# Kernel tuning notes

Measured on AMD Instinct MI355X. Metric: run time of the kernel, lower is better.

The kernel has to match this reference:

```python
import jax, jax.numpy as jnp
import numpy as np

NUM_HEADS = 16
NUM_GROUPS = 4
NUM_KV_HEADS = NUM_HEADS // NUM_GROUPS  # 4
HEAD_DIM = 64
MAX_DIST = 484


def setup_inputs() -> dict:
    key = jax.random.key(0)
    ks = jax.random.split(key, 8)
    B, S, E, H = 32, 484, 1024, 1024
    kv_dim = HEAD_DIM * NUM_GROUPS  # 256
    s_in = 0.03
    return {
        "query": jax.random.normal(ks[0], (B, S, E), dtype=jnp.float32),
        "key": jax.random.normal(ks[1], (B, S, E), dtype=jnp.float32),
        "value": jax.random.normal(ks[2], (B, S, E), dtype=jnp.float32),
        "Wq": jax.random.normal(ks[3], (E, H), dtype=jnp.float32) * s_in,
        "Wk": jax.random.normal(ks[4], (E, kv_dim), dtype=jnp.float32) * s_in,
        "Wv": jax.random.normal(ks[5], (E, kv_dim), dtype=jnp.float32) * s_in,
        "Wo": jax.random.normal(ks[6], (H, E), dtype=jnp.float32) * s_in,
        "rel_table": jax.random.normal(ks[7], (2 * MAX_DIST - 1, NUM_HEADS), dtype=jnp.float32) * 0.02,
    }


def _rel_bias(rel_table, q_len, k_len):
    # relative position k - q, clipped to [-(MD-1), MD-1], shifted to table index
    rel = jnp.arange(k_len)[None, :] - jnp.arange(q_len)[:, None]
    idx = jnp.clip(rel, -(MAX_DIST - 1), MAX_DIST - 1) + (MAX_DIST - 1)
    bias = rel_table[idx]  # [q, k, heads]
    return jnp.transpose(bias, (2, 0, 1))  # [heads, q, k]


def reference(query, key, value, Wq, Wk, Wv, Wo, rel_table):
    B, Q, _ = query.shape
    K = key.shape[1]
    G, Hkv, D = NUM_GROUPS, NUM_KV_HEADS, HEAD_DIM
    # projections; torch head split: head index = g*Hkv + h
    q = (query @ Wq).reshape(B, Q, G * Hkv, D).transpose(0, 2, 1, 3)
    q = q.reshape(B, G, Hkv, Q, D)  # b g h sq d
    k = (key @ Wk).reshape(B, K, G, D).transpose(0, 2, 1, 3)  # b g sk d
    v = (value @ Wv).reshape(B, K, G, D).transpose(0, 2, 1, 3)  # b g sv d
    scale = jnp.float32(D) ** 0.5
    scores = jnp.einsum('bghqd,bgkd->bghqk', q, k) / scale
    bias = _rel_bias(rel_table, Q, K).reshape(1, G, Hkv, Q, K)
    attn = jax.nn.softmax(scores + bias, axis=-1)
    out = jnp.einsum('bghqk,bgkd->bghqd', attn, v)
    out = out.reshape(B, G * Hkv, Q, D).transpose(0, 2, 1, 3).reshape(B, Q, G * Hkv * D)
    return out @ Wo
```

## Files before the change

### kernel.cpp

```cpp
#include <hip/hip_runtime.h>
#include <hip/hip_bf16.h>

typedef __attribute__((ext_vector_type(8))) short short8;
typedef __attribute__((ext_vector_type(4))) float f32x4;
typedef __attribute__((ext_vector_type(4))) unsigned uintx4;

#define B_  32
#define S_  484
#define E_  1024
#define NH  16
#define SP  512
#define M_  (B_*S_)

static __device__ __forceinline__ ushort f2bf(float f) {
  union { float f; unsigned u; } v; v.f = f;
  unsigned u = v.u;
  return (ushort)((u + 0x7FFFu + ((u >> 16) & 1u)) >> 16);
}

static __device__ __forceinline__ unsigned cvt_pk_bf16(float lo, float hi) {
  unsigned r;
  asm("v_cvt_pk_bf16_f32 %0, %1, %2" : "=v"(r) : "v"(lo), "v"(hi));
  return r;
}

#define GLOAD_LDS16(gp, lp) \
  __builtin_amdgcn_global_load_lds((const __attribute__((address_space(1))) void*)(gp), \
                                   (__attribute__((address_space(3))) void*)(lp), 16, 0, 0)

__global__ __launch_bounds__(256)
void transpose_convert(const float* __restrict__ W, ushort* __restrict__ WT, int K, int N) {
  __shared__ float tile[32][33];
  int k0 = blockIdx.y * 32, n0 = blockIdx.x * 32;
  int tx = threadIdx.x, ty = threadIdx.y;
  for (int i = ty; i < 32; i += 8) tile[i][tx] = W[(size_t)(k0 + i) * N + n0 + tx];
  __syncthreads();
  for (int i = ty; i < 32; i += 8) WT[(size_t)(n0 + i) * K + k0 + tx] = f2bf(tile[tx][i]);
}

template<int EPI, int SWZ, int AF32, int NXLOG>
__global__ __launch_bounds__(256)
void gemm_bt(const void* __restrict__ Ain, const ushort* __restrict__ BT,
             void* __restrict__ Cout, int N, int K, int HN, float oscale) {
  __shared__ alignas(16) ushort sA[2][128 * 32];
  __shared__ alignas(16) ushort sB[2][128 * 32];
  const int tid = threadIdx.x;
  const int lane = tid & 63, w = tid >> 6;

  const int nwg = gridDim.x;
  const int qq = nwg >> 3, rr = nwg & 7;
  const int x = blockIdx.x & 7, seq = blockIdx.x >> 3;
  const int logical = x * qq + (x < rr ? x : rr) + seq;
  const int m0 = (logical >> NXLOG) * 128;
  const int n0 = (logical & ((1 << NXLOG) - 1)) * 128;
  const int NK = K >> 5;

  const int srow = w * 32 + (lane >> 2);
  const int scol = (lane & 3) * 8;
  const ushort* gB0 = BT + (size_t)(n0 + srow) * K + scol;

  const ushort* gA0bf = (const ushort*)Ain + (size_t)(m0 + srow) * K + scol;
  const int arow = w * 32 + (lane >> 1);
  const int acol = (lane & 1) * 16;
  const float* gA0f = (const float*)Ain + (size_t)(m0 + arow) * K + acol;

  const int wr = w >> 1, wc = w & 1;
  const int g4 = lane >> 4, l16 = lane & 15;
  const int aoff = (wr * 64 + l16) * 32 + 8 * g4;
  const int boff = (wc * 64 + l16) * 32 + 8 * g4;

  f32x4 acc[4][4] = {};
  float4 fA0, fA1, fA2, fA3;

  auto issueA = [&](int kt) {
    const float4* p = (const float4*)(gA0f + kt * 32);
    fA0 = p[0]; fA1 = p[1]; fA2 = p[2]; fA3 = p[3];
  };
  auto writeA = [&](int buf) {
    unsigned d0 = cvt_pk_bf16(fA0.x, fA0.y), d1 = cvt_pk_bf16(fA0.z, fA0.w);
    unsigned d2 = cvt_pk_bf16(fA1.x, fA1.y), d3 = cvt_pk_bf16(fA1.z, fA1.w);
    unsigned d4 = cvt_pk_bf16(fA2.x, fA2.y), d5 = cvt_pk_bf16(fA2.z, fA2.w);
    unsigned d6 = cvt_pk_bf16(fA3.x, fA3.y), d7 = cvt_pk_bf16(fA3.z, fA3.w);
    ushort* dst = &sA[buf][arow * 32 + acol];
    uintx4 q0 = {d0, d1, d2, d3}, q1 = {d4, d5, d6, d7};
    *(uintx4*)dst = q0;
    *(uintx4*)(dst + 8) = q1;
  };

  if (AF32) issueA(0);
  else {
    GLOAD_LDS16(gA0bf,          &sA[0][(w * 32) * 32]);
    GLOAD_LDS16(gA0bf + 16 * K, &sA[0][(w * 32 + 16) * 32]);
  }
  GLOAD_LDS16(gB0,          &sB[0][(w * 32) * 32]);
  GLOAD_LDS16(gB0 + 16 * K, &sB[0][(w * 32 + 16) * 32]);
  if (AF32) writeA(0);

  for (int kt = 0; kt < NK; ++kt) {
    __syncthreads();
    const int nb = (kt + 1) & 1;
    if (kt + 1 < NK) {
      const ushort* gb = gB0 + (kt + 1) * 32;
      GLOAD_LDS16(gb,          &sB[nb][(w * 32) * 32]);
      GLOAD_LDS16(gb + 16 * K, &sB[nb][(w * 32 + 16) * 32]);
      if (AF32) issueA(kt + 1);
      else {
        const ushort* ga = gA0bf + (kt + 1) * 32;
        GLOAD_LDS16(ga,          &sA[nb][(w * 32) * 32]);
        GLOAD_LDS16(ga + 16 * K, &sA[nb][(w * 32 + 16) * 32]);
      }
    }
    const ushort* pa = &sA[kt & 1][aoff];
    const ushort* pb = &sB[kt & 1][boff];
    short8 af[4], bf[4];
#pragma unroll
    for (int i = 0; i < 4; ++i) {
      af[i] = *(const short8*)(pa + i * 16 * 32);
      bf[i] = *(const short8*)(pb + i * 16 * 32);
    }
#pragma unroll
    for (int mi = 0; mi < 4; ++mi)
#pragma unroll
      for (int ni = 0; ni < 4; ++ni)
        acc[mi][ni] = __builtin_amdgcn_mfma_f32_16x16x32_bf16(af[mi], bf[ni], acc[mi][ni], 0, 0, 0);
    if (AF32 && kt + 1 < NK) writeA(nb);
  }

#pragma unroll
  for (int mi = 0; mi < 4; ++mi) {
#pragma unroll
    for (int ni = 0; ni < 4; ++ni) {
#pragma unroll
      for (int r = 0; r < 4; ++r) {
        int m = m0 + wr * 64 + mi * 16 + g4 * 4 + r;
        int n = n0 + wc * 64 + ni * 16 + l16;
        float vv = acc[mi][ni][r];
        if (EPI == 2) {
          ((float*)Cout)[(size_t)m * N + n] = vv;
        } else {
          int b = m / S_, pos = m % S_;
          if (EPI == 0) {
            int dd = n & 63;
            if (SWZ) dd ^= (pos & 7) << 3;
            ushort hv = f2bf(vv * oscale);
            ((ushort*)Cout)[(((size_t)b * HN + (n >> 6)) * SP + pos) * 64 + dd] = hv;
          } else {
            int local = pos & 31;
            int j = (local < 16) ? (2 * local) : (2 * local - 31);
            int pf_ = (pos & ~31) | (j ^ ((n & 3) << 3));
            ushort hv = f2bf(vv);
            ((ushort*)Cout)[(((size_t)b * HN + (n >> 6)) * 64 + (n & 63)) * SP + pf_] = hv;
          }
        }
      }
    }
  }
}

__global__ __launch_bounds__(256)
void attn_kernel(const ushort* __restrict__ qp, const ushort* __restrict__ kp,
                 const ushort* __restrict__ vpT, const float* __restrict__ rel,
                 ushort* __restrict__ ao) {
  __shared__ float sBias[1056];
  __shared__ alignas(16) ushort sK[2][32 * 64];
  __shared__ alignas(16) ushort sV[2][64 * 32];
  __shared__ alignas(16) ushort sP[4][16 * 40];
  const int tid = threadIdx.x;
  const int blk = blockIdx.x;
  const int logical = (blk & 7) * 512 + (blk >> 3);
  const int qt = logical & 7, head = (logical >> 3) & 15, b = logical >> 7;
  const int g = head >> 2;
  const float LOG2E = 1.44269504f;
  for (int t = tid; t < 1056; t += 256)
    sBias[t] = (t >= 32 && t < 999) ? rel[(t - 32) * 16 + head] * LOG2E : -1e30f;

  const int lane = tid & 63, w = tid >> 6;
  const int g4 = lane >> 4, l16 = lane & 15;
  const int qw = qt * 64 + w * 16;

  const ushort* qbase = qp + (((size_t)b * NH + head) * SP + qw + l16) * 64;
  short8 qf0 = *(const short8*)(qbase + 8 * g4);
  short8 qf1 = *(const short8*)(qbase + 32 + 8 * g4);

  const ushort* kSrc = kp  + ((size_t)b * 4 + g) * SP * 64 + (tid >> 3) * 64 + (tid & 7) * 8;
  const ushort* vSrc = vpT + ((size_t)b * 4 + g) * 64 * SP + (tid >> 2) * SP + (tid & 3) * 8;

  f32x4 acc[4] = {};
  float ps[4] = {0.f, 0.f, 0.f, 0.f};
  const int ib = l16 - (qw + g4 * 4) + 483 + 32;
  ushort* sPw = &sP[w][0];

  const int kswz  = (l16 & 7) << 3;
  const int kOff0 = l16 * 64 + ((8 * g4) ^ kswz);
  const int kOff1 = l16 * 64 + ((32 + 8 * g4) ^ kswz);
  const int vOff  = l16 * 32 + 8 * (g4 ^ (l16 & 3));

  GLOAD_LDS16(kSrc, &sK[0][w * 512]);
  GLOAD_LDS16(vSrc, &sV[0][w * 512]);

  for (int kt = 0; kt < 16; ++kt) {
    __syncthreads();
    if (kt + 1 < 16) {
      GLOAD_LDS16(kSrc + (kt + 1) * 2048, &sK[(kt + 1) & 1][w * 512]);
      GLOAD_LDS16(vSrc + (kt + 1) * 32,   &sV[(kt + 1) & 1][w * 512]);
    }
    const ushort* sk = &sK[kt & 1][0];
    const ushort* sv = &sV[kt & 1][0];
    short8 kf0 = *(const short8*)(sk + kOff0);
    short8 kf1 = *(const short8*)(sk + kOff1);
    short8 kf2 = *(const short8*)(sk + 1024 + kOff0);
    short8 kf3 = *(const short8*)(sk + 1024 + kOff1);
    f32x4 s0 = {}, s1 = {};
    s0 = __builtin_amdgcn_mfma_f32_16x16x32_bf16(qf0, kf0, s0, 0, 0, 0);
    s0 = __builtin_amdgcn_mfma_f32_16x16x32_bf16(qf1, kf1, s0, 0, 0, 0);
    s1 = __builtin_amdgcn_mfma_f32_16x16x32_bf16(qf0, kf2, s1, 0, 0, 0);
    s1 = __builtin_amdgcn_mfma_f32_16x16x32_bf16(qf1, kf3, s1, 0, 0, 0);

    const int k0 = kt * 32;
#pragma unroll
    for (int r = 0; r < 4; ++r) {
      int i0 = ib + k0 - r;
      float p0 = __builtin_amdgcn_exp2f(s0[r] + sBias[i0]);
      float p1 = __builtin_amdgcn_exp2f(s1[r] + sBias[i0 + 16]);
      if (kt == 15) {
        p0 = (k0 + l16 < S_) ? p0 : 0.f;
        p1 = (k0 + 16 + l16 < S_) ? p1 : 0.f;
      }
      ps[r] += p0 + p1;
      *(unsigned*)(sPw + (g4 * 4 + r) * 40 + 2 * l16) = cvt_pk_bf16(p0, p1);
    }
    short8 pf = *(const short8*)(sPw + l16 * 40 + 8 * g4);
#pragma unroll
    for (int nt = 0; nt < 4; ++nt) {
      short8 vf = *(const short8*)(sv + vOff + nt * 512);
      acc[nt] = __builtin_amdgcn_mfma_f32_16x16x32_bf16(pf, vf, acc[nt], 0, 0, 0);
    }
  }

#pragma unroll
  for (int off = 1; off < 16; off <<= 1) {
#pragma unroll
    for (int r = 0; r < 4; ++r) ps[r] += __shfl_xor(ps[r], off, 64);
  }

#pragma unroll
  for (int r = 0; r < 4; ++r) {
    int q_abs = qw + g4 * 4 + r;
    if (q_abs < S_) {
      float inv = 1.f / ps[r];
#pragma unroll
      for (int nt = 0; nt < 4; ++nt) {
        int dd = nt * 16 + l16;
        ao[((size_t)b * S_ + q_abs) * 1024 + head * 64 + dd] = f2bf(acc[nt][r] * inv);
      }
    }
  }
}

extern "C" void kernel_launch(void* const* d_in, const int* in_sizes, int n_in,
                              void* d_out, int out_size, void* d_ws, size_t ws_size,
                              hipStream_t stream) {
  const float* query = (const float*)d_in[0];
  const float* key   = (const float*)d_in[1];
  const float* value = (const float*)d_in[2];
  const float* Wq    = (const float*)d_in[3];
  const float* Wk    = (const float*)d_in[4];
  const float* Wv    = (const float*)d_in[5];
  const float* Wo    = (const float*)d_in[6];
  const float* rel   = (const float*)d_in[7];

  char* ws = (char*)d_ws;
  size_t off = 0;
  auto alloc = [&](size_t bytes) { char* p = ws + off; off += (bytes + 255) & ~(size_t)255; return p; };

  const size_t MEelems = (size_t)M_ * E_;
  ushort* wqT = (ushort*)alloc((size_t)1024 * 1024 * 2);
  ushort* wkT = (ushort*)alloc((size_t)256 * 1024 * 2);
  ushort* wvT = (ushort*)alloc((size_t)256 * 1024 * 2);
  ushort* woT = (ushort*)alloc((size_t)1024 * 1024 * 2);
  ushort* qp  = (ushort*)alloc((size_t)B_ * NH * SP * 64 * 2);
  ushort* kp  = (ushort*)alloc((size_t)B_ * 4 * SP * 64 * 2);
  ushort* vp  = (ushort*)alloc((size_t)B_ * 4 * 64 * SP * 2);
  ushort* ao  = (ushort*)alloc(MEelems * 2);

  transpose_convert<<<dim3(32, 32), dim3(32, 8), 0, stream>>>(Wq, wqT, 1024, 1024);
  transpose_convert<<<dim3(8, 32),  dim3(32, 8), 0, stream>>>(Wk, wkT, 1024, 256);
  transpose_convert<<<dim3(8, 32),  dim3(32, 8), 0, stream>>>(Wv, wvT, 1024, 256);
  transpose_convert<<<dim3(32, 32), dim3(32, 8), 0, stream>>>(Wo, woT, 1024, 1024);

  const float QSCALE = 0.125f * 1.44269504f;
  gemm_bt<0,0,1,3><<<968, 256, 0, stream>>>(query, wqT, qp, 1024, 1024, NH, QSCALE);
  gemm_bt<0,1,1,1><<<242, 256, 0, stream>>>(key,   wkT, kp, 256, 1024, 4, 1.0f);
  gemm_bt<1,1,1,1><<<242, 256, 0, stream>>>(value, wvT, vp, 256, 1024, 4, 1.0f);

  attn_kernel<<<4096, 256, 0, stream>>>(qp, kp, vp, rel, ao);

  gemm_bt<2,0,0,3><<<968, 256, 0, stream>>>(ao, woT, d_out, 1024, 1024, 0, 1.0f);
}
```

Baseline: 305.6 us.

## Use 256x256-tile GEMM kernel with 512 threads for Q and output projections

Adds a gemm_big kernel that computes 256x256 output tiles with 8 waves, each holding an 8x4 grid of MFMA accumulators, and uses it for the Q projection and the output projection. Larger tiles cut global and LDS traffic per FLOP and halve the redundant fp32 A reloads. The cost is 244 workgroups on a 256-CU device, higher register pressure from 128 accumulator floats per lane, and a partial last M tile that needs bounds checks. The EPI==2 branch is dropped from gemm_bt because it is no longer used.

New measurement: 301.8 us. About the same (-1.2%).

```diff
diff --git a/kernel.cpp b/kernel.cpp
--- a/kernel.cpp
+++ b/kernel.cpp
@@ -36,6 +36,106 @@
   for (int i = ty; i < 32; i += 8) tile[i][tx] = W[(size_t)(k0 + i) * N + n0 + tx];
   __syncthreads();
   for (int i = ty; i < 32; i += 8) WT[(size_t)(n0 + i) * K + k0 + tx] = f2bf(tile[tx][i]);
+}
+
+template<int EPI, int AF32>
+__global__ __launch_bounds__(512)
+void gemm_big(const void* __restrict__ Ain, const ushort* __restrict__ BT,
+              void* __restrict__ Cout, float oscale) {
+  const int K = 1024, N = 1024, NK = 32;
+  __shared__ alignas(16) ushort sA[2][256 * 32];
+  __shared__ alignas(16) ushort sB[2][256 * 32];
+  const int tid = threadIdx.x;
+  const int lane = tid & 63, w = tid >> 6;
+  const int m0 = (blockIdx.x >> 2) * 256;
+  const int n0 = (blockIdx.x & 3) * 256;
+
+  const int brow = tid >> 2, bcol = (tid & 3) * 8;
+  const ushort* gB0 = BT + (size_t)(n0 + brow) * K + bcol;
+  const int dstB = tid * 8;
+
+  const int rowA0 = min(m0 + brow, M_ - 1);
+  const int rowA1 = min(m0 + brow + 128, M_ - 1);
+  const ushort* gA0bf = (const ushort*)Ain + (size_t)rowA0 * K + bcol;
+  const ushort* gA1bf = (const ushort*)Ain + (size_t)rowA1 * K + bcol;
+
+  const int rowAf = min(m0 + (tid >> 1), M_ - 1);
+  const float* gA0f = (const float*)Ain + (size_t)rowAf * K + (tid & 1) * 16;
+  const int dstAf = (tid >> 1) * 32 + (tid & 1) * 16;
+
+  const int wr = w >> 2, wc = w & 3;
+  const int g4 = lane >> 4, l16 = lane & 15;
+
+  f32x4 acc[8][4] = {};
+  float4 fA0, fA1, fA2, fA3;
+
+  auto issueA = [&](int kt) {
+    const float4* p = (const float4*)(gA0f + kt * 32);
+    fA0 = p[0]; fA1 = p[1]; fA2 = p[2]; fA3 = p[3];
+  };
+  auto writeA = [&](int buf) {
+    unsigned d0 = cvt_pk_bf16(fA0.x, fA0.y), d1 = cvt_pk_bf16(fA0.z, fA0.w);
+    unsigned d2 = cvt_pk_bf16(fA1.x, fA1.y), d3 = cvt_pk_bf16(fA1.z, fA1.w);
+    unsigned d4 = cvt_pk_bf16(fA2.x, fA2.y), d5 = cvt_pk_bf16(fA2.z, fA2.w);
+    unsigned d6 = cvt_pk_bf16(fA3.x, fA3.y), d7 = cvt_pk_bf16(fA3.z, fA3.w);
+    ushort* dst = &sA[buf][dstAf];
+    uintx4 q0 = {d0, d1, d2, d3}, q1 = {d4, d5, d6, d7};
+    *(uintx4*)dst = q0;
+    *(uintx4*)(dst + 8) = q1;
+  };
+  auto stage = [&](int kt, int buf) {
+    GLOAD_LDS16(gB0 + kt * 32,           &sB[buf][dstB]);
+    GLOAD_LDS16(gB0 + kt * 32 + 128 * K, &sB[buf][dstB + 4096]);
+    if (AF32) issueA(kt);
+    else {
+      GLOAD_LDS16(gA0bf + kt * 32, &sA[buf][dstB]);
+      GLOAD_LDS16(gA1bf + kt * 32, &sA[buf][dstB + 4096]);
+    }
+  };
+
+  stage(0, 0);
+  if (AF32) writeA(0);
+
+  for (int kt = 0; kt < NK; ++kt) {
+    __syncthreads();
+    const int nb = (kt + 1) & 1;
+    if (kt + 1 < NK) stage(kt + 1, nb);
+    const ushort* pa = &sA[kt & 1][(wr * 128 + l16) * 32 + 8 * g4];
+    const ushort* pb = &sB[kt & 1][(wc * 64 + l16) * 32 + 8 * g4];
+    short8 af[8], bf[4];
+#pragma unroll
+    for (int i = 0; i < 8; ++i) af[i] = *(const short8*)(pa + i * 16 * 32);
+#pragma unroll
+    for (int i = 0; i < 4; ++i) bf[i] = *(const short8*)(pb + i * 16 * 32);
+#pragma unroll
+    for (int mi = 0; mi < 8; ++mi)
+#pragma unroll
+      for (int ni = 0; ni < 4; ++ni)
+        acc[mi][ni] = __builtin_amdgcn_mfma_f32_16x16x32_bf16(af[mi], bf[ni], acc[mi][ni], 0, 0, 0);
+    if (AF32 && kt + 1 < NK) writeA(nb);
+  }
+
+#pragma unroll
+  for (int mi = 0; mi < 8; ++mi) {
+#pragma unroll
+    for (int ni = 0; ni < 4; ++ni) {
+#pragma unroll
+      for (int r = 0; r < 4; ++r) {
+        int m = m0 + wr * 128 + mi * 16 + g4 * 4 + r;
+        int n = n0 + wc * 64 + ni * 16 + l16;
+        if (m < M_) {
+          float vv = acc[mi][ni][r];
+          if (EPI == 2) {
+            ((float*)Cout)[(size_t)m * N + n] = vv;
+          } else {
+            int b = m / S_, pos = m % S_;
+            ushort hv = f2bf(vv * oscale);
+            ((ushort*)Cout)[(((size_t)b * NH + (n >> 6)) * SP + pos) * 64 + (n & 63)] = hv;
+          }
+        }
+      }
+    }
+  }
 }
 
 template<int EPI, int SWZ, int AF32, int NXLOG>
@@ -135,22 +235,18 @@
         int m = m0 + wr * 64 + mi * 16 + g4 * 4 + r;
         int n = n0 + wc * 64 + ni * 16 + l16;
         float vv = acc[mi][ni][r];
-        if (EPI == 2) {
-          ((float*)Cout)[(size_t)m * N + n] = vv;
+        int b = m / S_, pos = m % S_;
+        if (EPI == 0) {
+          int dd = n & 63;
+          if (SWZ) dd ^= (pos & 7) << 3;
+          ushort hv = f2bf(vv * oscale);
+          ((ushort*)Cout)[(((size_t)b * HN + (n >> 6)) * SP + pos) * 64 + dd] = hv;
         } else {
-          int b = m / S_, pos = m % S_;
-          if (EPI == 0) {
-            int dd = n & 63;
-            if (SWZ) dd ^= (pos & 7) << 3;
-            ushort hv = f2bf(vv * oscale);
-            ((ushort*)Cout)[(((size_t)b * HN + (n >> 6)) * SP + pos) * 64 + dd] = hv;
-          } else {
-            int local = pos & 31;
-            int j = (local < 16) ? (2 * local) : (2 * local - 31);
-            int pf_ = (pos & ~31) | (j ^ ((n & 3) << 3));
-            ushort hv = f2bf(vv);
-            ((ushort*)Cout)[(((size_t)b * HN + (n >> 6)) * 64 + (n & 63)) * SP + pf_] = hv;
-          }
+          int local = pos & 31;
+          int j = (local < 16) ? (2 * local) : (2 * local - 31);
+          int pf_ = (pos & ~31) | (j ^ ((n & 3) << 3));
+          ushort hv = f2bf(vv);
+          ((ushort*)Cout)[(((size_t)b * HN + (n >> 6)) * 64 + (n & 63)) * SP + pf_] = hv;
         }
       }
     }
@@ -289,11 +385,11 @@
   transpose_convert<<<dim3(32, 32), dim3(32, 8), 0, stream>>>(Wo, woT, 1024, 1024);
 
   const float QSCALE = 0.125f * 1.44269504f;
-  gemm_bt<0,0,1,3><<<968, 256, 0, stream>>>(query, wqT, qp, 1024, 1024, NH, QSCALE);
+  gemm_big<0,1><<<244, 512, 0, stream>>>(query, wqT, qp, QSCALE);
   gemm_bt<0,1,1,1><<<242, 256, 0, stream>>>(key,   wkT, kp, 256, 1024, 4, 1.0f);
   gemm_bt<1,1,1,1><<<242, 256, 0, stream>>>(value, wvT, vp, 256, 1024, 4, 1.0f);
 
   attn_kernel<<<4096, 256, 0, stream>>>(qp, kp, vp, rel, ao);
 
-  gemm_bt<2,0,0,3><<<968, 256, 0, stream>>>(ao, woT, d_out, 1024, 1024, 0, 1.0f);
-}
+  gemm_big<2,0><<<244, 512, 0, stream>>>(ao, woT, d_out, 1.0f);
+}
```

## Pre-convert query to bf16 and use triple-buffered async-LDS GEMM for Q and output projections

Applied to the files above, without the earlier changes.

Adds a standalone kernel that converts the fp32 query activations to bf16. The Q projection and output projection then run in a new GEMM that loads both operands with global_load_lds into a three-stage LDS ring, with explicit vmcnt waits, so loads run two tiles ahead of compute. The aim is to take the fp32 load and register conversion off the Q GEMM's critical path and to deepen prefetch. In exchange the query tensor takes an extra full fp32 read and bf16 write-back (about 60MB plus 30MB of traffic), and LDS use rises to 48KB per block, which may lower occupancy.

New measurement: 297.4 us. 2.7% less time.

```diff
diff --git a/kernel.cpp b/kernel.cpp
--- a/kernel.cpp
+++ b/kernel.cpp
@@ -27,6 +27,18 @@
 #define GLOAD_LDS16(gp, lp) \
   __builtin_amdgcn_global_load_lds((const __attribute__((address_space(1))) void*)(gp), \
                                    (__attribute__((address_space(3))) void*)(lp), 16, 0, 0)
+
+__global__ __launch_bounds__(256)
+void cvt_f32_bf16(const float* __restrict__ x, ushort* __restrict__ y, int n4) {
+  int i = blockIdx.x * 256 + threadIdx.x;
+  int stride = gridDim.x * 256;
+  for (; i < n4; i += stride) {
+    float4 v = ((const float4*)x)[i];
+    ushort4 h;
+    h.x = f2bf(v.x); h.y = f2bf(v.y); h.z = f2bf(v.z); h.w = f2bf(v.w);
+    ((ushort4*)y)[i] = h;
+  }
+}
 
 __global__ __launch_bounds__(256)
 void transpose_convert(const float* __restrict__ W, ushort* __restrict__ WT, int K, int N) {
@@ -38,12 +50,12 @@
   for (int i = ty; i < 32; i += 8) WT[(size_t)(n0 + i) * K + k0 + tx] = f2bf(tile[tx][i]);
 }
 
-template<int EPI, int SWZ, int AF32, int NXLOG>
-__global__ __launch_bounds__(256)
-void gemm_bt(const void* __restrict__ Ain, const ushort* __restrict__ BT,
-             void* __restrict__ Cout, int N, int K, int HN, float oscale) {
-  __shared__ alignas(16) ushort sA[2][128 * 32];
-  __shared__ alignas(16) ushort sB[2][128 * 32];
+template<int EPI, int NXLOG>
+__global__ __launch_bounds__(256)
+void gemm_cnt(const ushort* __restrict__ A, const ushort* __restrict__ BT,
+              void* __restrict__ Cout, int N, int K, float oscale) {
+  __shared__ alignas(16) ushort sA[3][128 * 32];
+  __shared__ alignas(16) ushort sB[3][128 * 32];
   const int tid = threadIdx.x;
   const int lane = tid & 63, w = tid >> 6;
 
@@ -57,12 +69,99 @@
 
   const int srow = w * 32 + (lane >> 2);
   const int scol = (lane & 3) * 8;
+  const ushort* gA0 = A  + (size_t)(m0 + srow) * K + scol;
   const ushort* gB0 = BT + (size_t)(n0 + srow) * K + scol;
 
-  const ushort* gA0bf = (const ushort*)Ain + (size_t)(m0 + srow) * K + scol;
+  const int wr = w >> 1, wc = w & 1;
+  const int g4 = lane >> 4, l16 = lane & 15;
+  const int aoff = (wr * 64 + l16) * 32 + 8 * g4;
+  const int boff = (wc * 64 + l16) * 32 + 8 * g4;
+
+  f32x4 acc[4][4] = {};
+
+  auto stage = [&](int kt, int buf) {
+    const ushort* ga = gA0 + kt * 32;
+    const ushort* gb = gB0 + kt * 32;
+    GLOAD_LDS16(ga,          &sA[buf][(w * 32) * 32]);
+    GLOAD_LDS16(ga + 16 * K, &sA[buf][(w * 32 + 16) * 32]);
+    GLOAD_LDS16(gb,          &sB[buf][(w * 32) * 32]);
+    GLOAD_LDS16(gb + 16 * K, &sB[buf][(w * 32 + 16) * 32]);
+  };
+
+  stage(0, 0);
+  stage(1, 1);
+
+  int cur = 0;
+  for (int kt = 0; kt < NK; ++kt) {
+    if (kt + 1 < NK) asm volatile("s_waitcnt vmcnt(4)" ::: "memory");
+    else             asm volatile("s_waitcnt vmcnt(0)" ::: "memory");
+    asm volatile("s_waitcnt lgkmcnt(0)" ::: "memory");
+    __builtin_amdgcn_s_barrier();
+    if (kt + 2 < NK) {
+      int nb = cur + 2; if (nb >= 3) nb -= 3;
+      stage(kt + 2, nb);
+    }
+    const ushort* pa = &sA[cur][aoff];
+    const ushort* pb = &sB[cur][boff];
+    short8 af[4], bf[4];
+#pragma unroll
+    for (int i = 0; i < 4; ++i) {
+      af[i] = *(const short8*)(pa + i * 16 * 32);
+      bf[i] = *(const short8*)(pb + i * 16 * 32);
+    }
+#pragma unroll
+    for (int mi = 0; mi < 4; ++mi)
+#pragma unroll
+      for (int ni = 0; ni < 4; ++ni)
+        acc[mi][ni] = __builtin_amdgcn_mfma_f32_16x16x32_bf16(af[mi], bf[ni], acc[mi][ni], 0, 0, 0);
+    if (++cur >= 3) cur = 0;
+  }
+
+#pragma unroll
+  for (int mi = 0; mi < 4; ++mi) {
+#pragma unroll
+    for (int ni = 0; ni < 4; ++ni) {
+#pragma unroll
+      for (int r = 0; r < 4; ++r) {
+        int m = m0 + wr * 64 + mi * 16 + g4 * 4 + r;
+        int n = n0 + wc * 64 + ni * 16 + l16;
+        float vv = acc[mi][ni][r];
+        if (EPI == 2) {
+          ((float*)Cout)[(size_t)m * N + n] = vv;
+        } else {
+          int b = m / S_, pos = m % S_;
+          ushort hv = f2bf(vv * oscale);
+          ((ushort*)Cout)[(((size_t)b * NH + (n >> 6)) * SP + pos) * 64 + (n & 63)] = hv;
+        }
+      }
+    }
+  }
+}
+
+template<int EPI, int SWZ, int NXLOG>
+__global__ __launch_bounds__(256)
+void gemm_bt(const float* __restrict__ Ain, const ushort* __restrict__ BT,
+             void* __restrict__ Cout, int N, int K, int HN, float oscale) {
+  __shared__ alignas(16) ushort sA[2][128 * 32];
+  __shared__ alignas(16) ushort sB[2][128 * 32];
+  const int tid = threadIdx.x;
+  const int lane = tid & 63, w = tid >> 6;
+
+  const int nwg = gridDim.x;
+  const int qq = nwg >> 3, rr = nwg & 7;
+  const int x = blockIdx.x & 7, seq = blockIdx.x >> 3;
+  const int logical = x * qq + (x < rr ? x : rr) + seq;
+  const int m0 = (logical >> NXLOG) * 128;
+  const int n0 = (logical & ((1 << NXLOG) - 1)) * 128;
+  const int NK = K >> 5;
+
+  const int srow = w * 32 + (lane >> 2);
+  const int scol = (lane & 3) * 8;
+  const ushort* gB0 = BT + (size_t)(n0 + srow) * K + scol;
+
   const int arow = w * 32 + (lane >> 1);
   const int acol = (lane & 1) * 16;
-  const float* gA0f = (const float*)Ain + (size_t)(m0 + arow) * K + acol;
+  const float* gA0f = Ain + (size_t)(m0 + arow) * K + acol;
 
   const int wr = w >> 1, wc = w & 1;
   const int g4 = lane >> 4, l16 = lane & 15;
@@ -87,14 +186,10 @@
     *(uintx4*)(dst + 8) = q1;
   };
 
-  if (AF32) issueA(0);
-  else {
-    GLOAD_LDS16(gA0bf,          &sA[0][(w * 32) * 32]);
-    GLOAD_LDS16(gA0bf + 16 * K, &sA[0][(w * 32 + 16) * 32]);
-  }
+  issueA(0);
   GLOAD_LDS16(gB0,          &sB[0][(w * 32) * 32]);
   GLOAD_LDS16(gB0 + 16 * K, &sB[0][(w * 32 + 16) * 32]);
-  if (AF32) writeA(0);
+  writeA(0);
 
   for (int kt = 0; kt < NK; ++kt) {
     __syncthreads();
@@ -103,12 +198,7 @@
       const ushort* gb = gB0 + (kt + 1) * 32;
       GLOAD_LDS16(gb,          &sB[nb][(w * 32) * 32]);
       GLOAD_LDS16(gb + 16 * K, &sB[nb][(w * 32 + 16) * 32]);
-      if (AF32) issueA(kt + 1);
-      else {
-        const ushort* ga = gA0bf + (kt + 1) * 32;
-        GLOAD_LDS16(ga,          &sA[nb][(w * 32) * 32]);
-        GLOAD_LDS16(ga + 16 * K, &sA[nb][(w * 32 + 16) * 32]);
-      }
+      issueA(kt + 1);
     }
     const ushort* pa = &sA[kt & 1][aoff];
     const ushort* pb = &sB[kt & 1][boff];
@@ -123,7 +213,7 @@
 #pragma unroll
       for (int ni = 0; ni < 4; ++ni)
         acc[mi][ni] = __builtin_amdgcn_mfma_f32_16x16x32_bf16(af[mi], bf[ni], acc[mi][ni], 0, 0, 0);
-    if (AF32 && kt + 1 < NK) writeA(nb);
+    if (kt + 1 < NK) writeA(nb);
   }
 
 #pragma unroll
@@ -135,22 +225,18 @@
         int m = m0 + wr * 64 + mi * 16 + g4 * 4 + r;
         int n = n0 + wc * 64 + ni * 16 + l16;
         float vv = acc[mi][ni][r];
-        if (EPI == 2) {
-          ((float*)Cout)[(size_t)m * N + n] = vv;
+        int b = m / S_, pos = m % S_;
+        if (EPI == 0) {
+          int dd = n & 63;
+          if (SWZ) dd ^= (pos & 7) << 3;
+          ushort hv = f2bf(vv * oscale);
+          ((ushort*)Cout)[(((size_t)b * HN + (n >> 6)) * SP + pos) * 64 + dd] = hv;
         } else {
-          int b = m / S_, pos = m % S_;
-          if (EPI == 0) {
-            int dd = n & 63;
-            if (SWZ) dd ^= (pos & 7) << 3;
-            ushort hv = f2bf(vv * oscale);
-            ((ushort*)Cout)[(((size_t)b * HN + (n >> 6)) * SP + pos) * 64 + dd] = hv;
-          } else {
-            int local = pos & 31;
-            int j = (local < 16) ? (2 * local) : (2 * local - 31);
-            int pf_ = (pos & ~31) | (j ^ ((n & 3) << 3));
-            ushort hv = f2bf(vv);
-            ((ushort*)Cout)[(((size_t)b * HN + (n >> 6)) * 64 + (n & 63)) * SP + pf_] = hv;
-          }
+          int local = pos & 31;
+          int j = (local < 16) ? (2 * local) : (2 * local - 31);
+          int pf_ = (pos & ~31) | (j ^ ((n & 3) << 3));
+          ushort hv = f2bf(vv);
+          ((ushort*)Cout)[(((size_t)b * HN + (n >> 6)) * 64 + (n & 63)) * SP + pf_] = hv;
         }
       }
     }
@@ -274,6 +360,7 @@
   auto alloc = [&](size_t bytes) { char* p = ws + off; off += (bytes + 255) & ~(size_t)255; return p; };
 
   const size_t MEelems = (size_t)M_ * E_;
+  ushort* qb  = (ushort*)alloc(MEelems * 2);
   ushort* wqT = (ushort*)alloc((size_t)1024 * 1024 * 2);
   ushort* wkT = (ushort*)alloc((size_t)256 * 1024 * 2);
   ushort* wvT = (ushort*)alloc((size_t)256 * 1024 * 2);
@@ -283,17 +370,19 @@
   ushort* vp  = (ushort*)alloc((size_t)B_ * 4 * 64 * SP * 2);
   ushort* ao  = (ushort*)alloc(MEelems * 2);
 
+  cvt_f32_bf16<<<2048, 256, 0, stream>>>(query, qb, (int)(MEelems / 4));
+
   transpose_convert<<<dim3(32, 32), dim3(32, 8), 0, stream>>>(Wq, wqT, 1024, 1024);
   transpose_convert<<<dim3(8, 32),  dim3(32, 8), 0, stream>>>(Wk, wkT, 1024, 256);
   transpose_convert<<<dim3(8, 32),  dim3(32, 8), 0, stream>>>(Wv, wvT, 1024, 256);
   transpose_convert<<<dim3(32, 32), dim3(32, 8), 0, stream>>>(Wo, woT, 1024, 1024);
 
   const float QSCALE = 0.125f * 1.44269504f;
-  gemm_bt<0,0,1,3><<<968, 256, 0, stream>>>(query, wqT, qp, 1024, 1024, NH, QSCALE);
-  gemm_bt<0,1,1,1><<<242, 256, 0, stream>>>(key,   wkT, kp, 256, 1024, 4, 1.0f);
-  gemm_bt<1,1,1,1><<<242, 256, 0, stream>>>(value, wvT, vp, 256, 1024, 4, 1.0f);
+  gemm_cnt<0,3><<<968, 256, 0, stream>>>(qb, wqT, qp, 1024, 1024, QSCALE);
+  gemm_bt<0,1,1><<<242, 256, 0, stream>>>(key,   wkT, kp, 256, 1024, 4, 1.0f);
+  gemm_bt<1,1,1><<<242, 256, 0, stream>>>(value, wvT, vp, 256, 1024, 4, 1.0f);
 
   attn_kernel<<<4096, 256, 0, stream>>>(qp, kp, vp, rel, ao);
 
-  gemm_bt<2,0,0,3><<<968, 256, 0, stream>>>(ao, woT, d_out, 1024, 1024, 0, 1.0f);
-}
+  gemm_cnt<2,3><<<968, 256, 0, stream>>>(ao, woT, d_out, 1024, 1024, 1.0f);
+}
```
